# Performance work log

Hardware: AMD Instinct MI355X
Metric: run time of the kernel (lower is better)

## Reference

```python
import jax, jax.numpy as jnp
import numpy as np
import math

NUM_HEADS = 16

def _skew(QEr):
    # QEr: [B, H, S, S] -> pad 1 on left of last dim, reshape, drop first row
    B, H, S, _ = QEr.shape
    padded = jnp.pad(QEr, ((0, 0), (0, 0), (0, 0), (1, 0)))  # [B,H,S,S+1]
    reshaped = padded.reshape(B, H, S + 1, S)
    return reshaped[:, :, 1:, :]  # [B,H,S,S]

def setup_inputs() -> dict:
    key = jax.random.key(0)
    ks = jax.random.split(key, 8)
    B, S, D, dh = 4, 1024, 1024, 64
    x = jax.random.normal(ks[0], (B, S, D), dtype=jnp.float32)
    scale = 1.0 / math.sqrt(D)
    Wq = jax.random.normal(ks[1], (D, D), dtype=jnp.float32) * scale
    Wk = jax.random.normal(ks[2], (D, D), dtype=jnp.float32) * scale
    Wv = jax.random.normal(ks[3], (D, D), dtype=jnp.float32) * scale
    bq = jnp.zeros((D,), dtype=jnp.float32)
    bk = jnp.zeros((D,), dtype=jnp.float32)
    bv = jnp.zeros((D,), dtype=jnp.float32)
    Er = jax.random.normal(ks[4], (S, dh), dtype=jnp.float32)
    return {"x": x, "Wq": Wq, "bq": bq, "Wk": Wk, "bk": bk, "Wv": Wv, "bv": bv, "Er": Er}

def reference(x, Wq, bq, Wk, bk, Wv, bv, Er):
    B, S, D = x.shape
    H = NUM_HEADS
    dh = D // H
    # Linear projections (torch Linear: x @ W.T + b)
    q = (x @ Wq.T + bq).reshape(B, S, H, dh).transpose(0, 2, 1, 3)  # [B,H,S,dh]
    k = (x @ Wk.T + bk).reshape(B, S, H, dh).transpose(0, 2, 1, 3)
    v = (x @ Wv.T + bv).reshape(B, S, H, dh).transpose(0, 2, 1, 3)
    # Relative position term: q @ Er^T then skew (start = max_len - S = 0)
    QEr = jnp.einsum('bhsd,td->bhst', q, Er)  # [B,H,S,S]
    Srel = _skew(QEr)
    QKt = jnp.einsum('bhsd,bhtd->bhst', q, k)  # [B,H,S,S]
    attn = (QKt + Srel) / math.sqrt(dh)
    causal = jnp.tril(jnp.ones((S, S), dtype=bool))
    attn = jnp.where(causal[None, None], attn, jnp.float32(-1e6))
    attn = jax.nn.softmax(attn, axis=-1)
    out = jnp.einsum('bhst,bhtd->bhsd', attn, v)  # [B,H,S,dh]
    out = out.transpose(0, 2, 1, 3).reshape(B, S, D)
    return out  # dropout is identity in eval / p=0
```

## Files before the change

kernel.cpp:

```cpp
#include <hip/hip_runtime.h>
#include <stdint.h>

#define S_LEN 1024
#define DM 1024
#define NH 16
#define DH 64
#define NB 4

typedef unsigned short u16;
typedef __attribute__((ext_vector_type(8))) short short8;
typedef __attribute__((ext_vector_type(4))) float f32x4;
typedef __attribute__((ext_vector_type(4))) unsigned int u32x4;
typedef __attribute__((ext_vector_type(4))) unsigned short u16x4;

__device__ __forceinline__ u16 f2bf(float f) {
  union { float f; unsigned int u; } c;
  c.f = f;
  unsigned int u = c.u;
  return (u16)((u + 0x7fffu + ((u >> 16) & 1u)) >> 16);
}

__device__ __forceinline__ void g2l16(const void* g, void* l) {
  __builtin_amdgcn_global_load_lds(
      (const __attribute__((address_space(1))) unsigned int*)(uintptr_t)g,
      (__attribute__((address_space(3))) unsigned int*)(uint32_t)(uintptr_t)l,
      16, 0, 0);
}

__device__ __forceinline__ float grp16_max(float v) {
  union { float f; int i; } c, o;
  c.f = v; o.i = __builtin_amdgcn_update_dpp(c.i, c.i, 0xB1, 0xF, 0xF, false);
  v = fmaxf(v, o.f);
  c.f = v; o.i = __builtin_amdgcn_update_dpp(c.i, c.i, 0x4E, 0xF, 0xF, false);
  v = fmaxf(v, o.f);
  c.f = v; o.i = __builtin_amdgcn_update_dpp(c.i, c.i, 0x124, 0xF, 0xF, false);
  v = fmaxf(v, o.f);
  c.f = v; o.i = __builtin_amdgcn_update_dpp(c.i, c.i, 0x128, 0xF, 0xF, false);
  v = fmaxf(v, o.f);
  return v;
}
__device__ __forceinline__ float grp16_sum(float v) {
  union { float f; int i; } c, o;
  c.f = v; o.i = __builtin_amdgcn_update_dpp(c.i, c.i, 0xB1, 0xF, 0xF, false);
  v += o.f;
  c.f = v; o.i = __builtin_amdgcn_update_dpp(c.i, c.i, 0x4E, 0xF, 0xF, false);
  v += o.f;
  c.f = v; o.i = __builtin_amdgcn_update_dpp(c.i, c.i, 0x124, 0xF, 0xF, false);
  v += o.f;
  c.f = v; o.i = __builtin_amdgcn_update_dpp(c.i, c.i, 0x128, 0xF, 0xF, false);
  v += o.f;
  return v;
}

__global__ __launch_bounds__(256) void cvt_f32_bf16(
    const float* __restrict__ x, const float* __restrict__ Wq,
    const float* __restrict__ Wk, const float* __restrict__ Wv,
    const float* __restrict__ Er, u16* __restrict__ xb,
    u16* __restrict__ Wqb, u16* __restrict__ Wkb, u16* __restrict__ Wvb,
    u16* __restrict__ Erb) {
  const size_t f = ((size_t)blockIdx.x * 256 + threadIdx.x) * 8;
  const float* src;
  u16* dst;
  size_t off;
  if (f < 4194304) { src = x; dst = xb; off = f; }
  else if (f < 5242880) { src = Wq; dst = Wqb; off = f - 4194304; }
  else if (f < 6291456) { src = Wk; dst = Wkb; off = f - 5242880; }
  else if (f < 7340032) { src = Wv; dst = Wvb; off = f - 6291456; }
  else { src = Er; dst = Erb; off = f - 7340032; }
  const float4 a = *(const float4*)(src + off);
  const float4 b = *(const float4*)(src + off + 4);
  u16 o[8] = {f2bf(a.x), f2bf(a.y), f2bf(a.z), f2bf(a.w),
              f2bf(b.x), f2bf(b.y), f2bf(b.z), f2bf(b.w)};
  *(u32x4*)(dst + off) = *(const u32x4*)o;
}

__global__ __launch_bounds__(256) void qkv_gemm(
    const u16* __restrict__ x,
    const u16* __restrict__ Wq, const float* __restrict__ bq,
    const u16* __restrict__ Wk, const float* __restrict__ bk,
    const u16* __restrict__ Wv, const float* __restrict__ bv,
    u16* __restrict__ Qo, u16* __restrict__ Ko, u16* __restrict__ Vo) {
  __shared__ __attribute__((aligned(16))) u16 Al[128 * 32];
  __shared__ __attribute__((aligned(16))) u16 Bl[128 * 32];

  const int tid = threadIdx.x;
  const int lane = tid & 63;
  const int wave = tid >> 6;

  const int o =
      ((int)blockIdx.z * gridDim.y + blockIdx.y) * gridDim.x + blockIdx.x;
  const int swz = (o & 7) * 96 + (o >> 3);
  const int z = swz >> 8;
  const int rem = swz & 255;
  const int m0 = (rem >> 3) * 128;
  const int n0 = (rem & 7) * 128;

  const u16* W = (z == 0) ? Wq : (z == 1) ? Wk : Wv;
  const float* bias = (z == 0) ? bq : (z == 1) ? bk : bv;

  f32x4 acc[4][4];
  const f32x4 fzero = {0.f, 0.f, 0.f, 0.f};
#pragma unroll
  for (int i = 0; i < 4; i++)
#pragma unroll
    for (int j = 0; j < 4; j++) acc[i][j] = fzero;

  const int srow = tid >> 2;
  const int schunk = tid & 3;
  const u16* gA = x + (size_t)(m0 + srow) * DM + schunk * 8;
  const u16* gB = W + (size_t)(n0 + srow) * DM + schunk * 8;

  const int fr = lane & 15;
  const int fq = lane >> 4;
  const int wr = (wave >> 1) * 64;
  const int wc = (wave & 1) * 64;

  for (int k = 0; k < DM; k += 32) {
    g2l16(gA + k, &Al[tid * 8]);
    g2l16(gA + (size_t)64 * DM + k, &Al[2048 + tid * 8]);
    g2l16(gB + k, &Bl[tid * 8]);
    g2l16(gB + (size_t)64 * DM + k, &Bl[2048 + tid * 8]);
    __syncthreads();
    short8 a[4], b[4];
#pragma unroll
    for (int i = 0; i < 4; i++)
      a[i] = *(const short8*)&Al[(wr + i * 16 + fr) * 32 + fq * 8];
#pragma unroll
    for (int j = 0; j < 4; j++)
      b[j] = *(const short8*)&Bl[(wc + j * 16 + fr) * 32 + fq * 8];
#pragma unroll
    for (int i = 0; i < 4; i++)
#pragma unroll
      for (int j = 0; j < 4; j++)
        acc[i][j] =
            __builtin_amdgcn_mfma_f32_16x16x32_bf16(a[i], b[j], acc[i][j], 0, 0, 0);
    __syncthreads();
  }

#pragma unroll
  for (int j = 0; j < 4; j++) {
    const int n = n0 + wc + j * 16 + fr;
    const float bsv = bias[n];
    const int h = n >> 6, d = n & (DH - 1);
#pragma unroll
    for (int i = 0; i < 4; i++) {
      const int mb = m0 + wr + i * 16 + fq * 4;
      const int bb = mb >> 10, s = mb & (S_LEN - 1);
      if (z == 2) {
        u16x4 ov;
#pragma unroll
        for (int r = 0; r < 4; r++) ov[r] = f2bf(acc[i][j][r] + bsv);
        *(u16x4*)&Vo[((size_t)(bb * NH + h) * DH + d) * S_LEN + s] = ov;
      } else if (z == 1) {
#pragma unroll
        for (int r = 0; r < 4; r++)
          Ko[((size_t)(bb * NH + h) * S_LEN + s + r) * DH + d] =
              f2bf(acc[i][j][r] + bsv);
      } else {
#pragma unroll
        for (int r = 0; r < 4; r++)
          Qo[((size_t)(bb * NH + h) * S_LEN + s + r) * DH + d] =
              f2bf(acc[i][j][r] + bsv);
      }
    }
  }
}

__global__ __launch_bounds__(512, 4) void attn(
    const u16* __restrict__ Q, const u16* __restrict__ K,
    const u16* __restrict__ Vt, const u16* __restrict__ Er,
    float* __restrict__ out) {
  __shared__ __attribute__((aligned(16))) u16 Kl[2][64 * 64];
  __shared__ __attribute__((aligned(16))) u16 Vl[2][64 * 64];
  __shared__ __attribute__((aligned(16))) u16 El[256 * 64];
  __shared__ __attribute__((aligned(16))) u16 Pl[8][16 * 64];

  const int tid = threadIdx.x;
  const int lane = tid & 63;
  const int w = tid >> 6;
  const int bh = blockIdx.y;
  const int b = bh >> 4, h = bh & (NH - 1);
  const int it = (bh < 32) ? (int)blockIdx.x : 7 - (int)blockIdx.x;
  const int i0 = it * 128;
  const int jmax = i0 + 64;
  const int i0w = i0 + w * 16;
  const int E0b = S_LEN - 128 - i0;

  const u16* Qb = Q + (size_t)bh * S_LEN * DH;
  const char* Kb = (const char*)(K + (size_t)bh * S_LEN * DH);
  const char* Vb = (const char*)(Vt + (size_t)bh * DH * S_LEN);
  const char* Eb = (const char*)Er;
  u16* Pw = Pl[w];

  const int fr = lane & 15;
  const int fq = lane >> 4;
  const f32x4 fzero = {0.f, 0.f, 0.f, 0.f};

  const int r0 = tid >> 3;
  const int ch = (tid & 7) * 16;

  auto stageKV = [&](int j0, int bf) {
    const int sw = ch ^ ((r0 & 7) << 4);
    g2l16(Kb + (size_t)(j0 + r0) * 128 + sw, (char*)&Kl[bf][0] + r0 * 128 + ch);
    g2l16(Vb + (size_t)r0 * 2048 + j0 * 2 + sw,
          (char*)&Vl[bf][0] + r0 * 128 + ch);
  };
  auto stageEl = [&](int e0, int np) {
    for (int p = 0; p < np; p++) {
      const int e = e0 + p * 64 + r0;
      const int slot = e & 255;
      const int ec = (e > S_LEN - 1) ? (S_LEN - 1) : e;
      const int sw = ch ^ ((slot & 7) << 4);
      g2l16(Eb + (size_t)ec * 128 + sw, (char*)El + slot * 128 + ch);
    }
  };

  const short8 aq0 = *(const short8*)&Qb[(size_t)(i0w + fr) * DH + fq * 8];
  const short8 aq1 = *(const short8*)&Qb[(size_t)(i0w + fr) * DH + 32 + fq * 8];

  float mrow[4], lp[4];
  f32x4 accO[4];
#pragma unroll
  for (int r = 0; r < 4; r++) { mrow[r] = -3.0e38f; lp[r] = 0.f; }
#pragma unroll
  for (int t = 0; t < 4; t++) accO[t] = fzero;

  f32x4 zzc = fzero;
  const int ksw = (fr & 7) << 4;

  int buf = 0;
  stageKV(0, 0);
  stageEl(E0b, 3);
  __syncthreads();

  for (int j0 = 0; j0 <= jmax; j0 += 64) {
    if (j0 < jmax) {
      stageKV(j0 + 64, buf ^ 1);
      stageEl(E0b + j0 + 192, 1);
    }

    int tmax = (i0w + 15 - j0) >> 4;
    if (tmax > 3) tmax = 3;

    if (tmax >= 0) {
      f32x4 sfr[4];
#pragma unroll
      for (int t = 0; t < 4; t++) sfr[t] = fzero;
      __builtin_amdgcn_s_setprio(1);
#pragma unroll
      for (int t = 0; t < 4; t++)
        if (t <= tmax) {
          const char* kr = (const char*)&Kl[buf][0] + (t * 16 + fr) * 128;
          const short8 b0 = *(const short8*)(kr + ((fq * 16) ^ ksw));
          const short8 b1 = *(const short8*)(kr + ((64 + fq * 16) ^ ksw));
          f32x4 z = fzero;
          z = __builtin_amdgcn_mfma_f32_16x16x32_bf16(aq0, b0, z, 0, 0, 0);
          z = __builtin_amdgcn_mfma_f32_16x16x32_bf16(aq1, b1, z, 0, 0, 0);
          sfr[t] = z;
        }
      __builtin_amdgcn_s_setprio(0);

      const int ebs = S_LEN - 16 - i0w + j0;
      f32x4 zz[5];
#pragma unroll
      for (int f = 0; f < 5; f++) zz[f] = fzero;
      const int f0 = (j0 == 0) ? 0 : 1;
#pragma unroll
      for (int f = 0; f < 5; f++)
        if (f >= f0 && f <= tmax + 1) {
          const int slot = ((ebs + f * 16) & 255) + fr;
          const char* er = (const char*)El + slot * 128;
          const short8 b0 = *(const short8*)(er + ((fq * 16) ^ ksw));
          const short8 b1 = *(const short8*)(er + ((64 + fq * 16) ^ ksw));
          f32x4 z = fzero;
          z = __builtin_amdgcn_mfma_f32_16x16x32_bf16(aq0, b0, z, 0, 0, 0);
          z = __builtin_amdgcn_mfma_f32_16x16x32_bf16(aq1, b1, z, 0, 0, 0);
          zz[f] = z;
        }
      if (j0 > 0) zz[0] = zzc;
      zzc = zz[4];

      float p[4][4];
#pragma unroll
      for (int r = 0; r < 4; r++) {
        const int row = fq * 4 + r;
        const int c = 15 - row + fr;
        const int src = (fq << 4) | (c & 15);
        float sh[5];
#pragma unroll
        for (int f = 0; f < 5; f++) sh[f] = __shfl(zz[f][r], src);
#pragma unroll
        for (int t = 0; t < 4; t++) {
          const float rel = (c < 16) ? sh[t] : sh[t + 1];
          float sv = (sfr[t][r] + rel) * 0.125f;
          const int jj = j0 + t * 16 + fr;
          const int ii = i0w + row;
          if (jj > ii) sv = -3.0e38f;
          p[t][r] = sv;
        }
      }

#pragma unroll
      for (int r = 0; r < 4; r++) {
        float rm = fmaxf(fmaxf(p[0][r], p[1][r]), fmaxf(p[2][r], p[3][r]));
        rm = grp16_max(rm);
        const float mnew = fmaxf(mrow[r], rm);
        const float alpha = __expf(mrow[r] - mnew);
        mrow[r] = mnew;
        float rs = 0.f;
#pragma unroll
        for (int t = 0; t < 4; t++) {
          const float e = __expf(p[t][r] - mnew);
          p[t][r] = e;
          rs += e;
        }
        lp[r] = lp[r] * alpha + rs;
#pragma unroll
        for (int t = 0; t < 4; t++) accO[t][r] *= alpha;
      }

#pragma unroll
      for (int t = 0; t < 4; t++)
#pragma unroll
        for (int r = 0; r < 4; r++)
          Pw[(fq * 4 + r) * 64 + (((t ^ fq) << 4) + fr)] = f2bf(p[t][r]);
      __builtin_amdgcn_s_waitcnt(0xC07F);

      const int rsw = (fr >> 2) << 4;
      const short8 ap0 = *(const short8*)&Pw[fr * 64 + ((fq * 8) ^ rsw)];
      const short8 ap1 = *(const short8*)&Pw[fr * 64 + ((32 + fq * 8) ^ rsw)];

      __builtin_amdgcn_s_setprio(1);
#pragma unroll
      for (int t = 0; t < 4; t++) {
        const char* vr = (const char*)&Vl[buf][0] + (t * 16 + fr) * 128;
        const short8 b0 = *(const short8*)(vr + ((fq * 16) ^ ksw));
        const short8 b1 = *(const short8*)(vr + ((64 + fq * 16) ^ ksw));
        accO[t] =
            __builtin_amdgcn_mfma_f32_16x16x32_bf16(ap0, b0, accO[t], 0, 0, 0);
        accO[t] =
            __builtin_amdgcn_mfma_f32_16x16x32_bf16(ap1, b1, accO[t], 0, 0, 0);
      }
      __builtin_amdgcn_s_setprio(0);
    }

    __syncthreads();
    buf ^= 1;
  }

#pragma unroll
  for (int r = 0; r < 4; r++) {
    const float lr = grp16_sum(lp[r]);
    const float inv = 1.f / lr;
    const int s = i0w + fq * 4 + r;
#pragma unroll
    for (int t = 0; t < 4; t++) {
      const int d = t * 16 + fr;
      out[((size_t)b * S_LEN + s) * DM + h * DH + d] = accO[t][r] * inv;
    }
  }
}

extern "C" void kernel_launch(void* const* d_in, const int* in_sizes, int n_in,
                              void* d_out, int out_size, void* d_ws, size_t ws_size,
                              hipStream_t stream) {
  const float* x = (const float*)d_in[0];
  const float* Wq = (const float*)d_in[1];
  const float* bq = (const float*)d_in[2];
  const float* Wk = (const float*)d_in[3];
  const float* bk = (const float*)d_in[4];
  const float* Wv = (const float*)d_in[5];
  const float* bv = (const float*)d_in[6];
  const float* Er = (const float*)d_in[7];
  float* out = (float*)d_out;

  const size_t per = (size_t)NB * NH * S_LEN * DH;
  u16* Qw = (u16*)d_ws;
  u16* Kw = Qw + per;
  u16* Vw = Kw + per;
  u16* xb = Vw + per;
  u16* Wqb = xb + per;
  u16* Wkb = Wqb + (size_t)DM * DM;
  u16* Wvb = Wkb + (size_t)DM * DM;
  u16* Erb = Wvb + (size_t)DM * DM;

  cvt_f32_bf16<<<3616, 256, 0, stream>>>(x, Wq, Wk, Wv, Er, xb, Wqb, Wkb, Wvb,
                                         Erb);
  dim3 g1(DM / 128, (NB * S_LEN) / 128, 3);
  qkv_gemm<<<g1, dim3(256), 0, stream>>>(xb, Wqb, bq, Wkb, bk, Wvb, bv, Qw, Kw,
                                         Vw);
  dim3 g2(8, NB * NH);
  attn<<<g2, dim3(512), 0, stream>>>(Qw, Kw, Vw, Erb, out);
}
```

Baseline: 175.8 us.

## Double-buffer QKV GEMM LDS tiles and remap attention block-to-work assignment

```diff
diff --git a/kernel.cpp b/kernel.cpp
--- a/kernel.cpp
+++ b/kernel.cpp
@@ -80,8 +80,8 @@
     const u16* __restrict__ Wk, const float* __restrict__ bk,
     const u16* __restrict__ Wv, const float* __restrict__ bv,
     u16* __restrict__ Qo, u16* __restrict__ Ko, u16* __restrict__ Vo) {
-  __shared__ __attribute__((aligned(16))) u16 Al[128 * 32];
-  __shared__ __attribute__((aligned(16))) u16 Bl[128 * 32];
+  __shared__ __attribute__((aligned(16))) u16 Al[2][128 * 32];
+  __shared__ __attribute__((aligned(16))) u16 Bl[2][128 * 32];
 
   const int tid = threadIdx.x;
   const int lane = tid & 63;
@@ -115,26 +115,36 @@
   const int wr = (wave >> 1) * 64;
   const int wc = (wave & 1) * 64;
 
+  auto stageAB = [&](int k, int bf) {
+    g2l16(gA + k, &Al[bf][tid * 8]);
+    g2l16(gA + (size_t)64 * DM + k, &Al[bf][2048 + tid * 8]);
+    g2l16(gB + k, &Bl[bf][tid * 8]);
+    g2l16(gB + (size_t)64 * DM + k, &Bl[bf][2048 + tid * 8]);
+  };
+
+  stageAB(0, 0);
+  __syncthreads();
+  int bf = 0;
+
   for (int k = 0; k < DM; k += 32) {
-    g2l16(gA + k, &Al[tid * 8]);
-    g2l16(gA + (size_t)64 * DM + k, &Al[2048 + tid * 8]);
-    g2l16(gB + k, &Bl[tid * 8]);
-    g2l16(gB + (size_t)64 * DM + k, &Bl[2048 + tid * 8]);
-    __syncthreads();
+    if (k + 32 < DM) stageAB(k + 32, bf ^ 1);
     short8 a[4], b[4];
 #pragma unroll
     for (int i = 0; i < 4; i++)
-      a[i] = *(const short8*)&Al[(wr + i * 16 + fr) * 32 + fq * 8];
+      a[i] = *(const short8*)&Al[bf][(wr + i * 16 + fr) * 32 + fq * 8];
 #pragma unroll
     for (int j = 0; j < 4; j++)
-      b[j] = *(const short8*)&Bl[(wc + j * 16 + fr) * 32 + fq * 8];
+      b[j] = *(const short8*)&Bl[bf][(wc + j * 16 + fr) * 32 + fq * 8];
+    __builtin_amdgcn_s_setprio(1);
 #pragma unroll
     for (int i = 0; i < 4; i++)
 #pragma unroll
       for (int j = 0; j < 4; j++)
         acc[i][j] =
             __builtin_amdgcn_mfma_f32_16x16x32_bf16(a[i], b[j], acc[i][j], 0, 0, 0);
+    __builtin_amdgcn_s_setprio(0);
     __syncthreads();
+    bf ^= 1;
   }
 
 #pragma unroll
@@ -178,9 +188,10 @@
   const int tid = threadIdx.x;
   const int lane = tid & 63;
   const int w = tid >> 6;
-  const int bh = blockIdx.y;
+  const int bh = (int)blockIdx.x * 8 + ((int)blockIdx.y & 7);
+  const int slot = (int)blockIdx.y >> 3;
+  const int it = (slot < 4) ? slot : 11 - slot;
   const int b = bh >> 4, h = bh & (NH - 1);
-  const int it = (bh < 32) ? (int)blockIdx.x : 7 - (int)blockIdx.x;
   const int i0 = it * 128;
   const int jmax = i0 + 64;
   const int i0w = i0 + w * 16;
@@ -208,10 +219,10 @@
   auto stageEl = [&](int e0, int np) {
     for (int p = 0; p < np; p++) {
       const int e = e0 + p * 64 + r0;
-      const int slot = e & 255;
+      const int slt = e & 255;
       const int ec = (e > S_LEN - 1) ? (S_LEN - 1) : e;
-      const int sw = ch ^ ((slot & 7) << 4);
-      g2l16(Eb + (size_t)ec * 128 + sw, (char*)El + slot * 128 + ch);
+      const int sw = ch ^ ((slt & 7) << 4);
+      g2l16(Eb + (size_t)ec * 128 + sw, (char*)El + slt * 128 + ch);
     }
   };
 
@@ -268,8 +279,8 @@
 #pragma unroll
       for (int f = 0; f < 5; f++)
         if (f >= f0 && f <= tmax + 1) {
-          const int slot = ((ebs + f * 16) & 255) + fr;
-          const char* er = (const char*)El + slot * 128;
+          const int slt = ((ebs + f * 16) & 255) + fr;
+          const char* er = (const char*)El + slt * 128;
           const short8 b0 = *(const short8*)(er + ((fq * 16) ^ ksw));
           const short8 b1 = *(const short8*)(er + ((64 + fq * 16) ^ ksw));
           f32x4 z = fzero;
```

Result: faster. 161.4 us (-8.2%).
